# Kernel optimization log

Hardware: AMD Instinct MI355X
Metric: run time of the kernel (lower is better)

## Reference

```python
import jax, jax.numpy as jnp
import numpy as np

CAPACITY_FRAC = 0.5


def setup_inputs() -> dict:
    key = jax.random.key(0)
    ks = jax.random.split(key, 5)
    B, T, D, F = 4, 8192, 1024, 4096
    x = jax.random.normal(ks[0], (B, T, D), dtype=jnp.float32)
    w_router = jax.random.normal(ks[1], (D,), dtype=jnp.float32) / np.sqrt(D)
    w1 = jax.random.normal(ks[2], (D, F), dtype=jnp.float32) / np.sqrt(D)
    b1 = jnp.zeros((F,), dtype=jnp.float32)
    w2 = jax.random.normal(ks[3], (F, D), dtype=jnp.float32) / np.sqrt(F)
    b2 = jnp.zeros((D,), dtype=jnp.float32)
    return {"x": x, "w_router": w_router, "w1": w1, "b1": b1, "w2": w2, "b2": b2}


def _ffn_block(h, w1, b1, w2, b2):
    # standard transformer FFN wrapped by MixtureOfDepths
    return jax.nn.gelu(h @ w1 + b1) @ w2 + b2


def reference(x, w_router, w1, b1, w2, b2):
    B, T, D = x.shape
    capacity = max(1, int(T * CAPACITY_FRAC))
    # router: Linear(d_model, 1, bias=False) -> scores [B, T]
    scores = x @ w_router
    # top-k token selection per sequence
    _, tok_idx = jax.lax.top_k(scores, capacity)  # [B, capacity]
    # gather selected tokens: [B, capacity, D]
    selected = jnp.take_along_axis(x, tok_idx[:, :, None], axis=1)
    processed = _ffn_block(selected, w1, b1, w2, b2)
    # scatter processed tokens back into a copy of x (topk indices are unique per row)
    b_idx = jnp.arange(B)[:, None]
    out = x.at[b_idx, tok_idx].set(processed)
    return out
```

## Files before the change

kernel.cpp:

```cpp
#include <hip/hip_runtime.h>
#include <stdint.h>

typedef float v4f __attribute__((ext_vector_type(4)));
typedef short v8s __attribute__((ext_vector_type(8)));

constexpr int Bq = 4, Tq = 8192, Dq = 1024, Fq = 4096;
constexpr int CAP = Tq / 2;
constexpr int Mq  = Bq * CAP;

__device__ __forceinline__ unsigned short f2bf(float f) {
  unsigned int u = __float_as_uint(f);
  u += 0x7FFFu + ((u >> 16) & 1u);
  return (unsigned short)(u >> 16);
}

__device__ __forceinline__ void async_cp16(const void* g, void* l) {
  __builtin_amdgcn_global_load_lds(
      (__attribute__((address_space(1))) void*)g,
      (__attribute__((address_space(3))) void*)l, 16, 0, 0);
}

__global__ void scores_kernel(const float* __restrict__ x,
                              const float* __restrict__ wr_g,
                              double* __restrict__ scores) {
  __shared__ __align__(16) float wr[Dq];
  for (int i = threadIdx.x; i < Dq; i += 256) wr[i] = wr_g[i];
  __syncthreads();
  int wid = threadIdx.x >> 6, lane = threadIdx.x & 63;
  int gw = blockIdx.x * 4 + wid;
  const float4* wp = (const float4*)wr;
  for (int rr = 0; rr < 4; ++rr) {
    int row = gw * 4 + rr;
    const float4* xp = (const float4*)(x + (size_t)row * Dq);
    double s = 0.0;
#pragma unroll
    for (int q = 0; q < 4; ++q) {
      float4 v = xp[lane + q * 64];
      float4 w = wp[lane + q * 64];
      s += (double)v.x * w.x + (double)v.y * w.y + (double)v.z * w.z + (double)v.w * w.w;
    }
#pragma unroll
    for (int off = 32; off; off >>= 1) s += __shfl_down(s, off);
    if (lane == 0) scores[row] = s;
  }
}

__device__ __forceinline__ int block_reduce_i(int v, int* red, int tid) {
#pragma unroll
  for (int off = 32; off; off >>= 1) v += __shfl_down(v, off);
  __syncthreads();
  if ((tid & 63) == 0) red[tid >> 6] = v;
  __syncthreads();
  int s = 0;
#pragma unroll
  for (int k = 0; k < 16; ++k) s += red[k];
  return s;
}

__global__ __launch_bounds__(1024) void select_topk(const double* __restrict__ scores,
                                                    int* __restrict__ selIdx,
                                                    unsigned char* __restrict__ selFlag) {
  int b = blockIdx.x, tid = threadIdx.x;
  const double* s = scores + (size_t)b * Tq;
  __shared__ int red[16];
  __shared__ int counter;
  unsigned long long key[8];
#pragma unroll
  for (int i = 0; i < 8; ++i) {
    unsigned long long u = (unsigned long long)__double_as_longlong(s[tid + i * 1024]);
    key[i] = (u >> 63) ? ~u : (u | 0x8000000000000000ULL);
  }
  unsigned long long cutoff = 0ULL;
  for (int bit = 63; bit >= 0; --bit) {
    unsigned long long cand = cutoff | (1ULL << bit);
    int c = 0;
#pragma unroll
    for (int i = 0; i < 8; ++i) c += (key[i] >= cand) ? 1 : 0;
    int tot = block_reduce_i(c, red, tid);
    if (tot >= CAP) cutoff = cand;
  }
  int cGt = 0, cEq = 0;
#pragma unroll
  for (int i = 0; i < 8; ++i) { cGt += (key[i] > cutoff); cEq += (key[i] == cutoff); }
  int gtTot = block_reduce_i(cGt, red, tid);
  int eqTot = block_reduce_i(cEq, red, tid);
  int need = CAP - gtTot;
  if (tid == 0) counter = 0;
  __syncthreads();
  bool takeAllEq = (eqTot == need);
#pragma unroll
  for (int i = 0; i < 8; ++i) {
    int t = tid + i * 1024;
    bool sel = takeAllEq ? (key[i] >= cutoff) : (key[i] > cutoff);
    if (sel) { int pos = atomicAdd(&counter, 1); selIdx[b * CAP + pos] = t; }
    selFlag[(size_t)b * Tq + t] = sel ? (unsigned char)1 : (unsigned char)0;
  }
  if (!takeAllEq) {
    __syncthreads();
    if (tid == 0) {
      int taken = 0;
      for (int t = 0; t < Tq && taken < need; ++t) {
        unsigned long long u = (unsigned long long)__double_as_longlong(s[t]);
        unsigned long long k = (u >> 63) ? ~u : (u | 0x8000000000000000ULL);
        if (k == cutoff) {
          selIdx[b * CAP + gtTot + taken] = t;
          selFlag[(size_t)b * Tq + t] = 1;
          ++taken;
        }
      }
    }
  }
}

__global__ void gather_kernel(const float* __restrict__ x,
                              const int* __restrict__ selIdx,
                              unsigned short* __restrict__ Xs) {
  int wid = threadIdx.x >> 6, lane = threadIdx.x & 63;
  int m = blockIdx.x * 4 + wid;
  int b = m >> 12;
  int tok = selIdx[m];
  const float4* src = (const float4*)(x + ((size_t)b * Tq + tok) * Dq);
  ushort4* dst = (ushort4*)(Xs + (size_t)m * Dq);
#pragma unroll
  for (int q = 0; q < 4; ++q) {
    float4 v = src[lane + q * 64];
    ushort4 o; o.x = f2bf(v.x); o.y = f2bf(v.y); o.z = f2bf(v.z); o.w = f2bf(v.w);
    dst[lane + q * 64] = o;
  }
}

__global__ void copy_pass(const float* __restrict__ x,
                          const unsigned char* __restrict__ selFlag,
                          float* __restrict__ out) {
  int wid = threadIdx.x >> 6, lane = threadIdx.x & 63;
  int row = blockIdx.x * 4 + wid;
  if (selFlag[row]) return;
  const float4* src = (const float4*)(x + (size_t)row * Dq);
  float4* dst = (float4*)(out + (size_t)row * Dq);
#pragma unroll
  for (int q = 0; q < 4; ++q) dst[lane + q * 64] = src[lane + q * 64];
}

__global__ void transpose_f32_to_bf16(const float* __restrict__ in,
                                      unsigned short* __restrict__ out,
                                      int R, int C) {
  __shared__ float tile[32][33];
  int tx = threadIdx.x, ty = threadIdx.y;
  int c0 = blockIdx.x * 32, r0 = blockIdx.y * 32;
#pragma unroll
  for (int k = 0; k < 4; ++k)
    tile[ty + k * 8][tx] = in[(size_t)(r0 + ty + k * 8) * C + c0 + tx];
  __syncthreads();
#pragma unroll
  for (int k = 0; k < 4; ++k)
    out[(size_t)(c0 + ty + k * 8) * R + r0 + tx] = f2bf(tile[tx][ty + k * 8]);
}


__global__ __launch_bounds__(256) void gemm1_gelu(const unsigned short* __restrict__ A,
                                                  const unsigned short* __restrict__ Bt,
                                                  const float* __restrict__ bias,
                                                  unsigned short* __restrict__ H,
                                                  int nPanels) {
  constexpr int K = Dq, N = Fq;
  __shared__ __align__(16) unsigned short As[128 * 32];
  __shared__ __align__(16) unsigned short Bs[128 * 32];
  const int tid = threadIdx.x;
  const int wid = tid >> 6, lane = tid & 63;
  const int wm = wid >> 1, wn = wid & 1;
  const int quad = lane >> 4, l16 = lane & 15;

  int l = blockIdx.x;
  int pIdx, nIdx;
  if ((nPanels & 7) == 0) {
    nIdx = (l >> 3) & 31;
    pIdx = (l & 7) | ((l >> 8) << 3);
  } else {
    nIdx = l & 31;
    pIdx = l >> 5;
  }
  const int m0 = pIdx * 128, n0 = nIdx * 128;

  const int sRow = tid >> 2;
  const int sCol = (((tid & 3) ^ ((sRow >> 1) & 3)) << 3);
  const unsigned short* aG0 = A + (size_t)(m0 + sRow) * K + sCol;
  const unsigned short* aG1 = aG0 + (size_t)64 * K;
  const unsigned short* bG0 = Bt + (size_t)(n0 + sRow) * K + sCol;
  const unsigned short* bG1 = bG0 + (size_t)64 * K;
  unsigned short* aL0 = As + wid * 512;
  unsigned short* aL1 = As + 2048 + wid * 512;
  unsigned short* bL0 = Bs + wid * 512;
  unsigned short* bL1 = Bs + 2048 + wid * 512;

  const int swz = ((quad ^ ((l16 >> 1) & 3)) << 3);
  int aOff[4], bOff[4];
#pragma unroll
  for (int i = 0; i < 4; ++i) aOff[i] = (wm * 64 + i * 16 + l16) * 32 + swz;
#pragma unroll
  for (int j = 0; j < 4; ++j) bOff[j] = (wn * 64 + j * 16 + l16) * 32 + swz;

  v4f acc[4][4] = {};

  for (int k0 = 0; k0 < K; k0 += 32) {
    async_cp16(aG0 + k0, aL0);
    async_cp16(aG1 + k0, aL1);
    async_cp16(bG0 + k0, bL0);
    async_cp16(bG1 + k0, bL1);
    __syncthreads();
    v8s af[4], bfr[4];
#pragma unroll
    for (int i = 0; i < 4; ++i) af[i] = *(const v8s*)(As + aOff[i]);
#pragma unroll
    for (int j = 0; j < 4; ++j) bfr[j] = *(const v8s*)(Bs + bOff[j]);
#pragma unroll
    for (int i = 0; i < 4; ++i)
#pragma unroll
      for (int j = 0; j < 4; ++j)
        acc[i][j] = __builtin_amdgcn_mfma_f32_16x16x32_bf16(af[i], bfr[j], acc[i][j], 0, 0, 0);
    __syncthreads();
  }

  const int mBase = m0 + wm * 64, nBase = n0 + wn * 64;
  float bv[4];
#pragma unroll
  for (int j = 0; j < 4; ++j) bv[j] = bias[nBase + j * 16 + l16];
  const float kA = 0.7978845608028654f, kB = 0.044715f * 0.7978845608028654f;
  const float kE = -2.0f * 1.4426950408889634f;
#pragma unroll
  for (int i = 0; i < 4; ++i)
#pragma unroll
    for (int r = 0; r < 4; ++r) {
      const int row = mBase + i * 16 + quad * 4 + r;
      unsigned short* hp = H + (size_t)row * N;
#pragma unroll
      for (int j = 0; j < 4; ++j) {
        const int col = nBase + j * 16 + l16;
        float c = acc[i][j][r] + bv[j];
        float z = c * __builtin_fmaf(kB, c * c, kA);
        float a = exp2f(kE * fabsf(z));
        float th = copysignf((1.0f - a) * __builtin_amdgcn_rcpf(1.0f + a), z);
        hp[col] = f2bf(0.5f * c * (1.0f + th));
      }
    }
}

__global__ __launch_bounds__(256) void gemm2_scatter(const unsigned short* __restrict__ A,
                                                     const unsigned short* __restrict__ Bt,
                                                     const float* __restrict__ bias,
                                                     const int* __restrict__ selIdx,
                                                     float* __restrict__ out,
                                                     int chunkStart, int nPanels) {
  constexpr int K = Fq, N = Dq;
  __shared__ __align__(16) unsigned short As[128 * 32];
  __shared__ __align__(16) unsigned short Bs[128 * 32];
  const int tid = threadIdx.x;
  const int wid = tid >> 6, lane = tid & 63;
  const int wm = wid >> 1, wn = wid & 1;
  const int quad = lane >> 4, l16 = lane & 15;

  int l = blockIdx.x;
  int pIdx, nIdx;
  if ((nPanels & 7) == 0) {
    nIdx = (l >> 3) & 7;
    pIdx = (l & 7) | ((l >> 6) << 3);
  } else {
    nIdx = l & 7;
    pIdx = l >> 3;
  }
  const int m0 = pIdx * 128, n0 = nIdx * 128;

  const int sRow = tid >> 2;
  const int sCol = (((tid & 3) ^ ((sRow >> 1) & 3)) << 3);
  const unsigned short* aG0 = A + (size_t)(m0 + sRow) * K + sCol;
  const unsigned short* aG1 = aG0 + (size_t)64 * K;
  const unsigned short* bG0 = Bt + (size_t)(n0 + sRow) * K + sCol;
  const unsigned short* bG1 = bG0 + (size_t)64 * K;
  unsigned short* aL0 = As + wid * 512;
  unsigned short* aL1 = As + 2048 + wid * 512;
  unsigned short* bL0 = Bs + wid * 512;
  unsigned short* bL1 = Bs + 2048 + wid * 512;

  const int swz = ((quad ^ ((l16 >> 1) & 3)) << 3);
  int aOff[4], bOff[4];
#pragma unroll
  for (int i = 0; i < 4; ++i) aOff[i] = (wm * 64 + i * 16 + l16) * 32 + swz;
#pragma unroll
  for (int j = 0; j < 4; ++j) bOff[j] = (wn * 64 + j * 16 + l16) * 32 + swz;

  v4f acc[4][4] = {};

  for (int k0 = 0; k0 < K; k0 += 32) {
    async_cp16(aG0 + k0, aL0);
    async_cp16(aG1 + k0, aL1);
    async_cp16(bG0 + k0, bL0);
    async_cp16(bG1 + k0, bL1);
    __syncthreads();
    v8s af[4], bfr[4];
#pragma unroll
    for (int i = 0; i < 4; ++i) af[i] = *(const v8s*)(As + aOff[i]);
#pragma unroll
    for (int j = 0; j < 4; ++j) bfr[j] = *(const v8s*)(Bs + bOff[j]);
#pragma unroll
    for (int i = 0; i < 4; ++i)
#pragma unroll
      for (int j = 0; j < 4; ++j)
        acc[i][j] = __builtin_amdgcn_mfma_f32_16x16x32_bf16(af[i], bfr[j], acc[i][j], 0, 0, 0);
    __syncthreads();
  }

  const int mBase = m0 + wm * 64, nBase = n0 + wn * 64;
  float bv[4];
#pragma unroll
  for (int j = 0; j < 4; ++j) bv[j] = bias[nBase + j * 16 + l16];
#pragma unroll
  for (int i = 0; i < 4; ++i)
#pragma unroll
    for (int r = 0; r < 4; ++r) {
      const int lrow = mBase + i * 16 + quad * 4 + r;
      const int m = chunkStart + lrow;
      const int b = m >> 12;
      const int tok = selIdx[m];
      float* op = out + ((size_t)b * Tq + tok) * Dq;
#pragma unroll
      for (int j = 0; j < 4; ++j) {
        const int col = nBase + j * 16 + l16;
        op[col] = acc[i][j][r] + bv[j];
      }
    }
}

extern "C" void kernel_launch(void* const* d_in, const int* in_sizes, int n_in,
                              void* d_out, int out_size, void* d_ws, size_t ws_size,
                              hipStream_t stream) {
  const float* x        = (const float*)d_in[0];
  const float* w_router = (const float*)d_in[1];
  const float* w1       = (const float*)d_in[2];
  const float* b1       = (const float*)d_in[3];
  const float* w2       = (const float*)d_in[4];
  const float* b2       = (const float*)d_in[5];
  float* out = (float*)d_out;

  char* p = (char*)d_ws;
  auto alloc = [&](size_t bytes) {
    char* r = p;
    p += (bytes + 255) & ~(size_t)255;
    return r;
  };
  double* scores          = (double*)alloc((size_t)Bq * Tq * 8);
  int* selIdx             = (int*)alloc((size_t)Mq * 4);
  unsigned char* selFlag  = (unsigned char*)alloc((size_t)Bq * Tq);
  unsigned short* W1t     = (unsigned short*)alloc((size_t)Dq * Fq * 2);
  unsigned short* W2t     = (unsigned short*)alloc((size_t)Dq * Fq * 2);
  unsigned short* Xs      = (unsigned short*)alloc((size_t)Mq * Dq * 2);
  size_t used = (size_t)(p - (char*)d_ws);
  size_t rem = ws_size > used ? ws_size - used : 0;
  int chunkRows = (int)(rem / ((size_t)Fq * 2));
  chunkRows = (chunkRows / 128) * 128;
  if (chunkRows > Mq) chunkRows = Mq;
  if (chunkRows < 128) chunkRows = 128;
  unsigned short* H = (unsigned short*)p;

  transpose_f32_to_bf16<<<dim3(Fq / 32, Dq / 32), dim3(32, 8), 0, stream>>>(w1, W1t, Dq, Fq);
  transpose_f32_to_bf16<<<dim3(Dq / 32, Fq / 32), dim3(32, 8), 0, stream>>>(w2, W2t, Fq, Dq);
  scores_kernel<<<2048, 256, 0, stream>>>(x, w_router, scores);
  select_topk<<<Bq, 1024, 0, stream>>>(scores, selIdx, selFlag);
  gather_kernel<<<Mq / 4, 256, 0, stream>>>(x, selIdx, Xs);
  copy_pass<<<(Bq * Tq) / 4, 256, 0, stream>>>(x, selFlag, out);

  for (int r0 = 0; r0 < Mq; r0 += chunkRows) {
    int rows = (Mq - r0 < chunkRows) ? (Mq - r0) : chunkRows;
    int p1 = rows / 128;
    gemm1_gelu<<<32 * p1, 256, 0, stream>>>(Xs + (size_t)r0 * Dq, W1t, b1, H, p1);
    gemm2_scatter<<<8 * p1, 256, 0, stream>>>(H, W2t, b2, selIdx, out, r0, p1);
  }
}
```

Before: 698.9 us.

## Fuse prep kernels, radix-select top-k, merge gather/copy, simplify GELU

Merges both weight transposes and the router score computation into one launch, and combines the gather and the copy of unselected rows into a single pass driven by a per-token position map. Top-k selection now uses an 8-round byte radix histogram instead of a 64-step bitwise binary search with block reductions. The tanh-GELU epilogue is rewritten algebraically as c/(1+exp2(poly)), which drops the abs, copysign and an extra multiply. This removes launch overhead, one read of x, and many serial synchronisations in select, at the cost of shared-memory atomics and a branchy fused kernel.

```diff
diff --git a/kernel.cpp b/kernel.cpp
--- a/kernel.cpp
+++ b/kernel.cpp
@@ -20,28 +20,54 @@
       (__attribute__((address_space(3))) void*)l, 16, 0, 0);
 }
 
-__global__ void scores_kernel(const float* __restrict__ x,
-                              const float* __restrict__ wr_g,
-                              double* __restrict__ scores) {
-  __shared__ __align__(16) float wr[Dq];
-  for (int i = threadIdx.x; i < Dq; i += 256) wr[i] = wr_g[i];
-  __syncthreads();
-  int wid = threadIdx.x >> 6, lane = threadIdx.x & 63;
-  int gw = blockIdx.x * 4 + wid;
-  const float4* wp = (const float4*)wr;
-  for (int rr = 0; rr < 4; ++rr) {
-    int row = gw * 4 + rr;
-    const float4* xp = (const float4*)(x + (size_t)row * Dq);
-    double s = 0.0;
-#pragma unroll
-    for (int q = 0; q < 4; ++q) {
-      float4 v = xp[lane + q * 64];
-      float4 w = wp[lane + q * 64];
-      s += (double)v.x * w.x + (double)v.y * w.y + (double)v.z * w.z + (double)v.w * w.w;
-    }
-#pragma unroll
-    for (int off = 32; off; off >>= 1) s += __shfl_down(s, off);
-    if (lane == 0) scores[row] = s;
+__device__ __forceinline__ unsigned long long d2key(double d) {
+  unsigned long long u = (unsigned long long)__double_as_longlong(d);
+  return (u >> 63) ? ~u : (u | 0x8000000000000000ULL);
+}
+
+__global__ __launch_bounds__(256) void prep_kernel(const float* __restrict__ w1,
+                                                   const float* __restrict__ w2,
+                                                   unsigned short* __restrict__ W1t,
+                                                   unsigned short* __restrict__ W2t,
+                                                   const float* __restrict__ x,
+                                                   const float* __restrict__ wr_g,
+                                                   double* __restrict__ scores) {
+  __shared__ __align__(16) float smem[32 * 33];
+  const int bid = blockIdx.x;
+  if (bid < 8192) {
+    const int z = bid >> 12, t = bid & 4095;
+    const float* in; unsigned short* o; int R, C, c0, r0;
+    if (z == 0) { in = w1; o = W1t; R = Dq; C = Fq; c0 = (t & 127) * 32; r0 = (t >> 7) * 32; }
+    else        { in = w2; o = W2t; R = Fq; C = Dq; c0 = (t & 31) * 32;  r0 = (t >> 5) * 32; }
+    const int tx = threadIdx.x & 31, ty = threadIdx.x >> 5;
+#pragma unroll
+    for (int k = 0; k < 4; ++k)
+      smem[(ty + k * 8) * 33 + tx] = in[(size_t)(r0 + ty + k * 8) * C + c0 + tx];
+    __syncthreads();
+#pragma unroll
+    for (int k = 0; k < 4; ++k)
+      o[(size_t)(c0 + ty + k * 8) * R + r0 + tx] = f2bf(smem[tx * 33 + ty + k * 8]);
+  } else {
+    float* wr = smem;
+    for (int i = threadIdx.x; i < Dq; i += 256) wr[i] = wr_g[i];
+    __syncthreads();
+    const int wid = threadIdx.x >> 6, lane = threadIdx.x & 63;
+    const int gw = (bid - 8192) * 4 + wid;
+    const float4* wp = (const float4*)wr;
+    for (int rr = 0; rr < 4; ++rr) {
+      int row = gw * 4 + rr;
+      const float4* xp = (const float4*)(x + (size_t)row * Dq);
+      double s = 0.0;
+#pragma unroll
+      for (int q = 0; q < 4; ++q) {
+        float4 v = xp[lane + q * 64];
+        float4 w = wp[lane + q * 64];
+        s += (double)v.x * w.x + (double)v.y * w.y + (double)v.z * w.z + (double)v.w * w.w;
+      }
+#pragma unroll
+      for (int off = 32; off; off >>= 1) s += __shfl_down(s, off);
+      if (lane == 0) scores[row] = s;
+    }
   }
 }
 
@@ -59,52 +85,78 @@
 
 __global__ __launch_bounds__(1024) void select_topk(const double* __restrict__ scores,
                                                     int* __restrict__ selIdx,
-                                                    unsigned char* __restrict__ selFlag) {
-  int b = blockIdx.x, tid = threadIdx.x;
+                                                    int* __restrict__ selPos) {
+  const int b = blockIdx.x, tid = threadIdx.x;
+  const int wid = tid >> 6;
   const double* s = scores + (size_t)b * Tq;
+  __shared__ int hist[16 * 256];
+  __shared__ int tot[256];
+  __shared__ unsigned long long sh_prefix;
+  __shared__ int sh_remaining;
   __shared__ int red[16];
   __shared__ int counter;
+
   unsigned long long key[8];
 #pragma unroll
+  for (int i = 0; i < 8; ++i) key[i] = d2key(s[tid + i * 1024]);
+
+  if (tid == 0) { sh_prefix = 0ULL; sh_remaining = CAP; counter = 0; }
+  __syncthreads();
+
+  for (int r = 0; r < 8; ++r) {
+    const int shift = 56 - 8 * r;
+    for (int i = tid; i < 4096; i += 1024) hist[i] = 0;
+    __syncthreads();
+    const unsigned long long pmask = r ? (~0ULL << (64 - 8 * r)) : 0ULL;
+    const unsigned long long prefix = sh_prefix;
+#pragma unroll
+    for (int i = 0; i < 8; ++i)
+      if ((key[i] & pmask) == prefix)
+        atomicAdd(&hist[(wid << 8) + (int)((key[i] >> shift) & 255)], 1);
+    __syncthreads();
+    if (tid < 256) {
+      int t = 0;
+#pragma unroll
+      for (int w = 0; w < 16; ++w) t += hist[(w << 8) + tid];
+      tot[tid] = t;
+    }
+    __syncthreads();
+    if (tid == 0) {
+      int rem = sh_remaining, cum = 0, d = 255;
+      for (; d > 0; --d) { cum += tot[d]; if (cum >= rem) break; }
+      if (cum < rem) cum += tot[0];
+      sh_remaining = rem - (cum - tot[d]);
+      sh_prefix = prefix | ((unsigned long long)d << shift);
+    }
+    __syncthreads();
+  }
+  const unsigned long long cutoff = sh_prefix;
+
+  int cGt = 0, cEq = 0;
+#pragma unroll
+  for (int i = 0; i < 8; ++i) { cGt += (key[i] > cutoff); cEq += (key[i] == cutoff); }
+  const int gtTot = block_reduce_i(cGt, red, tid);
+  const int eqTot = block_reduce_i(cEq, red, tid);
+  const int need = CAP - gtTot;
+  __syncthreads();
+  const bool takeAllEq = (eqTot == need);
+#pragma unroll
   for (int i = 0; i < 8; ++i) {
-    unsigned long long u = (unsigned long long)__double_as_longlong(s[tid + i * 1024]);
-    key[i] = (u >> 63) ? ~u : (u | 0x8000000000000000ULL);
-  }
-  unsigned long long cutoff = 0ULL;
-  for (int bit = 63; bit >= 0; --bit) {
-    unsigned long long cand = cutoff | (1ULL << bit);
-    int c = 0;
-#pragma unroll
-    for (int i = 0; i < 8; ++i) c += (key[i] >= cand) ? 1 : 0;
-    int tot = block_reduce_i(c, red, tid);
-    if (tot >= CAP) cutoff = cand;
-  }
-  int cGt = 0, cEq = 0;
-#pragma unroll
-  for (int i = 0; i < 8; ++i) { cGt += (key[i] > cutoff); cEq += (key[i] == cutoff); }
-  int gtTot = block_reduce_i(cGt, red, tid);
-  int eqTot = block_reduce_i(cEq, red, tid);
-  int need = CAP - gtTot;
-  if (tid == 0) counter = 0;
-  __syncthreads();
-  bool takeAllEq = (eqTot == need);
-#pragma unroll
-  for (int i = 0; i < 8; ++i) {
-    int t = tid + i * 1024;
-    bool sel = takeAllEq ? (key[i] >= cutoff) : (key[i] > cutoff);
-    if (sel) { int pos = atomicAdd(&counter, 1); selIdx[b * CAP + pos] = t; }
-    selFlag[(size_t)b * Tq + t] = sel ? (unsigned char)1 : (unsigned char)0;
+    const int t = tid + i * 1024;
+    const bool sel = takeAllEq ? (key[i] >= cutoff) : (key[i] > cutoff);
+    int m = -1;
+    if (sel) { int pos = atomicAdd(&counter, 1); m = b * CAP + pos; selIdx[m] = t; }
+    selPos[(size_t)b * Tq + t] = m;
   }
   if (!takeAllEq) {
     __syncthreads();
     if (tid == 0) {
       int taken = 0;
       for (int t = 0; t < Tq && taken < need; ++t) {
-        unsigned long long u = (unsigned long long)__double_as_longlong(s[t]);
-        unsigned long long k = (u >> 63) ? ~u : (u | 0x8000000000000000ULL);
-        if (k == cutoff) {
-          selIdx[b * CAP + gtTot + taken] = t;
-          selFlag[(size_t)b * Tq + t] = 1;
+        if (d2key(s[t]) == cutoff) {
+          const int m = b * CAP + gtTot + taken;
+          selIdx[m] = t;
+          selPos[(size_t)b * Tq + t] = m;
           ++taken;
         }
       }
@@ -112,48 +164,27 @@
   }
 }
 
-__global__ void gather_kernel(const float* __restrict__ x,
-                              const int* __restrict__ selIdx,
-                              unsigned short* __restrict__ Xs) {
-  int wid = threadIdx.x >> 6, lane = threadIdx.x & 63;
-  int m = blockIdx.x * 4 + wid;
-  int b = m >> 12;
-  int tok = selIdx[m];
-  const float4* src = (const float4*)(x + ((size_t)b * Tq + tok) * Dq);
-  ushort4* dst = (ushort4*)(Xs + (size_t)m * Dq);
-#pragma unroll
-  for (int q = 0; q < 4; ++q) {
-    float4 v = src[lane + q * 64];
-    ushort4 o; o.x = f2bf(v.x); o.y = f2bf(v.y); o.z = f2bf(v.z); o.w = f2bf(v.w);
-    dst[lane + q * 64] = o;
-  }
-}
-
-__global__ void copy_pass(const float* __restrict__ x,
-                          const unsigned char* __restrict__ selFlag,
-                          float* __restrict__ out) {
-  int wid = threadIdx.x >> 6, lane = threadIdx.x & 63;
-  int row = blockIdx.x * 4 + wid;
-  if (selFlag[row]) return;
+__global__ void gather_copy(const float* __restrict__ x,
+                            const int* __restrict__ selPos,
+                            unsigned short* __restrict__ Xs,
+                            float* __restrict__ out) {
+  const int wid = threadIdx.x >> 6, lane = threadIdx.x & 63;
+  const int row = blockIdx.x * 4 + wid;
+  const int sp = selPos[row];
   const float4* src = (const float4*)(x + (size_t)row * Dq);
-  float4* dst = (float4*)(out + (size_t)row * Dq);
-#pragma unroll
-  for (int q = 0; q < 4; ++q) dst[lane + q * 64] = src[lane + q * 64];
-}
-
-__global__ void transpose_f32_to_bf16(const float* __restrict__ in,
-                                      unsigned short* __restrict__ out,
-                                      int R, int C) {
-  __shared__ float tile[32][33];
-  int tx = threadIdx.x, ty = threadIdx.y;
-  int c0 = blockIdx.x * 32, r0 = blockIdx.y * 32;
-#pragma unroll
-  for (int k = 0; k < 4; ++k)
-    tile[ty + k * 8][tx] = in[(size_t)(r0 + ty + k * 8) * C + c0 + tx];
-  __syncthreads();
-#pragma unroll
-  for (int k = 0; k < 4; ++k)
-    out[(size_t)(c0 + ty + k * 8) * R + r0 + tx] = f2bf(tile[tx][ty + k * 8]);
+  if (sp >= 0) {
+    ushort4* dst = (ushort4*)(Xs + (size_t)sp * Dq);
+#pragma unroll
+    for (int q = 0; q < 4; ++q) {
+      float4 v = src[lane + q * 64];
+      ushort4 o; o.x = f2bf(v.x); o.y = f2bf(v.y); o.z = f2bf(v.z); o.w = f2bf(v.w);
+      dst[lane + q * 64] = o;
+    }
+  } else {
+    float4* dst = (float4*)(out + (size_t)row * Dq);
+#pragma unroll
+    for (int q = 0; q < 4; ++q) dst[lane + q * 64] = src[lane + q * 64];
+  }
 }
 
 
@@ -224,8 +255,8 @@
   float bv[4];
 #pragma unroll
   for (int j = 0; j < 4; ++j) bv[j] = bias[nBase + j * 16 + l16];
-  const float kA = 0.7978845608028654f, kB = 0.044715f * 0.7978845608028654f;
-  const float kE = -2.0f * 1.4426950408889634f;
+  const float nA = -2.3022082f;
+  const float nB = -0.1029432f;
 #pragma unroll
   for (int i = 0; i < 4; ++i)
 #pragma unroll
@@ -236,10 +267,9 @@
       for (int j = 0; j < 4; ++j) {
         const int col = nBase + j * 16 + l16;
         float c = acc[i][j][r] + bv[j];
-        float z = c * __builtin_fmaf(kB, c * c, kA);
-        float a = exp2f(kE * fabsf(z));
-        float th = copysignf((1.0f - a) * __builtin_amdgcn_rcpf(1.0f + a), z);
-        hp[col] = f2bf(0.5f * c * (1.0f + th));
+        float y = c * __builtin_fmaf(nB, c * c, nA);
+        float t = exp2f(y);
+        hp[col] = f2bf(c * __builtin_amdgcn_rcpf(1.0f + t));
       }
     }
 }
@@ -346,12 +376,12 @@
     p += (bytes + 255) & ~(size_t)255;
     return r;
   };
-  double* scores          = (double*)alloc((size_t)Bq * Tq * 8);
-  int* selIdx             = (int*)alloc((size_t)Mq * 4);
-  unsigned char* selFlag  = (unsigned char*)alloc((size_t)Bq * Tq);
-  unsigned short* W1t     = (unsigned short*)alloc((size_t)Dq * Fq * 2);
-  unsigned short* W2t     = (unsigned short*)alloc((size_t)Dq * Fq * 2);
-  unsigned short* Xs      = (unsigned short*)alloc((size_t)Mq * Dq * 2);
+  double* scores      = (double*)alloc((size_t)Bq * Tq * 8);
+  int* selIdx         = (int*)alloc((size_t)Mq * 4);
+  int* selPos         = (int*)alloc((size_t)Bq * Tq * 4);
+  unsigned short* W1t = (unsigned short*)alloc((size_t)Dq * Fq * 2);
+  unsigned short* W2t = (unsigned short*)alloc((size_t)Dq * Fq * 2);
+  unsigned short* Xs  = (unsigned short*)alloc((size_t)Mq * Dq * 2);
   size_t used = (size_t)(p - (char*)d_ws);
   size_t rem = ws_size > used ? ws_size - used : 0;
   int chunkRows = (int)(rem / ((size_t)Fq * 2));
@@ -360,12 +390,9 @@
   if (chunkRows < 128) chunkRows = 128;
   unsigned short* H = (unsigned short*)p;
 
-  transpose_f32_to_bf16<<<dim3(Fq / 32, Dq / 32), dim3(32, 8), 0, stream>>>(w1, W1t, Dq, Fq);
-  transpose_f32_to_bf16<<<dim3(Dq / 32, Fq / 32), dim3(32, 8), 0, stream>>>(w2, W2t, Fq, Dq);
-  scores_kernel<<<2048, 256, 0, stream>>>(x, w_router, scores);
-  select_topk<<<Bq, 1024, 0, stream>>>(scores, selIdx, selFlag);
-  gather_kernel<<<Mq / 4, 256, 0, stream>>>(x, selIdx, Xs);
-  copy_pass<<<(Bq * Tq) / 4, 256, 0, stream>>>(x, selFlag, out);
+  prep_kernel<<<10240, 256, 0, stream>>>(w1, w2, W1t, W2t, x, w_router, scores);
+  select_topk<<<Bq, 1024, 0, stream>>>(scores, selIdx, selPos);
+  gather_copy<<<(Bq * Tq) / 4, 256, 0, stream>>>(x, selPos, Xs, out);
 
   for (int r0 = 0; r0 < Mq; r0 += chunkRows) {
     int rows = (Mq - r0 < chunkRows) ? (Mq - r0) : chunkRows;
```

After: 703.3 us. About the same (+0.6%).
